# Kernel optimization log

Hardware: AMD Instinct MI355X
Metric: run time of the kernel (lower is better)

## Reference

```python
import jax, jax.numpy as jnp
import numpy as np

# EISANI constants (inference path, dense non-EI weights, static connections)
NUM_BITS = 16        # EISANITABcontinuousVarEncodingNumBits
K_SYN = 32           # numberOfSynapsesPerSegment
SEGMENTS = 2         # numberOfSegmentsPerNeuron
THETA = 8            # segment activation threshold (synapse-count based)
H = 4096             # hiddenLayerSize
F = 128              # numberOfFeatures
C = 10               # numberOfClasses
B = 64               # batch


def _make_weight(key, h, s, p):
    """Dense weight [h, s, p] with exactly K_SYN nonzero +/-1 synapses per segment
    (mirrors _initialise_layer_weights dense non-EI branch)."""
    k1, k2 = jax.random.split(key)
    cols = jax.random.randint(k1, (h, s, K_SYN), 0, p)
    signs = jnp.where(jax.random.bernoulli(k2, 0.5, (h, s, K_SYN)), 1.0, -1.0).astype(jnp.float32)
    hh = jnp.arange(h)[:, None, None]
    ss = jnp.arange(s)[None, :, None]
    return jnp.zeros((h, s, p), jnp.float32).at[hh, ss, cols].set(signs)


def setup_inputs() -> dict:
    key = jax.random.key(0)
    kx, k0, k1, k2, ko = jax.random.split(key, 5)
    x = jax.random.uniform(kx, (B, F), dtype=jnp.float32)
    W0 = _make_weight(k0, H, SEGMENTS, F * NUM_BITS)
    W1 = _make_weight(k1, H, SEGMENTS, H)
    W2 = _make_weight(k2, H, SEGMENTS, H)
    outW = jax.random.normal(ko, (3, H, C), dtype=jnp.float32) * 0.02
    return {"x": x, "W0": W0, "W1": W1, "W2": W2, "outW": outW}


def _encode(x):
    # thermometer (graded) encoding of continuous vars into NUM_BITS binary bits
    thresholds = (jnp.arange(NUM_BITS, dtype=jnp.float32) + 1.0) / (NUM_BITS + 1.0)
    bits = (x[:, :, None] >= thresholds).astype(jnp.float32)  # [B, F, NUM_BITS]
    return bits.reshape(x.shape[0], -1)  # [B, F*NUM_BITS]


def reference(x, W0, W1, W2, outW):
    acts = _encode(x)  # [B, P0]
    layer_acts = []
    for W in (W0, W1, W2):
        # segment membrane sums over binary presynaptic activations
        z = jnp.einsum('bp,hsp->bhs', acts, W)  # [B, H, S]
        # neuron fires if ANY segment reaches threshold
        fired = jnp.any(z >= THETA, axis=-1)
        acts = fired.astype(jnp.float32)  # binary activation [B, H]
        layer_acts.append(acts)
    stacked = jnp.stack(layer_acts)  # [L, B, H]
    out = jnp.einsum('lbh,lhc->bc', stacked, outW)  # class scores [B, C]
    return out
```

## Files before the change

kernel.cpp:

```cpp
#include <hip/hip_runtime.h>
#include <hip/hip_bf16.h>

typedef unsigned long long u64;
typedef float f32x4 __attribute__((ext_vector_type(4)));

#define H_SZ 4096
#define NBITS 16
#define NFEAT 128
#define NCLS 10
#define THETA 8


__device__ __forceinline__ u64 bfly_stage(u64 x, int lane, int d, u64 Md) {
    u64 p = __shfl_xor(x, d);
    return (lane & d) ? ((x & Md) | ((p >> d) & ~Md))
                      : ((x & ~Md) | ((p << d) & Md));
}

__device__ __forceinline__ u64 transpose64(u64 x, int lane) {
    x = bfly_stage(x, lane, 32, 0xFFFFFFFF00000000ULL);
    x = bfly_stage(x, lane, 16, 0xFFFF0000FFFF0000ULL);
    x = bfly_stage(x, lane,  8, 0xFF00FF00FF00FF00ULL);
    x = bfly_stage(x, lane,  4, 0xF0F0F0F0F0F0F0F0ULL);
    x = bfly_stage(x, lane,  2, 0xCCCCCCCCCCCCCCCCULL);
    x = bfly_stage(x, lane,  1, 0xAAAAAAAAAAAAAAAAULL);
    return x;
}

__device__ __forceinline__ void chunk_accum(f32x4 a, f32x4 b, const u64* p,
                                            unsigned& zp0, unsigned& zn0,
                                            unsigned& zp1, unsigned& zn1) {
    u64 A0 = p[0], A1 = p[64], A2 = p[128], A3 = p[192];
    u64 m;
    m = __ballot(a.x > 0.0f); zp0 += __builtin_popcountll(A0 & m);
    m = __ballot(a.x < 0.0f); zn0 += __builtin_popcountll(A0 & m);
    m = __ballot(a.y > 0.0f); zp0 += __builtin_popcountll(A1 & m);
    m = __ballot(a.y < 0.0f); zn0 += __builtin_popcountll(A1 & m);
    m = __ballot(a.z > 0.0f); zp0 += __builtin_popcountll(A2 & m);
    m = __ballot(a.z < 0.0f); zn0 += __builtin_popcountll(A2 & m);
    m = __ballot(a.w > 0.0f); zp0 += __builtin_popcountll(A3 & m);
    m = __ballot(a.w < 0.0f); zn0 += __builtin_popcountll(A3 & m);

    m = __ballot(b.x > 0.0f); zp1 += __builtin_popcountll(A0 & m);
    m = __ballot(b.x < 0.0f); zn1 += __builtin_popcountll(A0 & m);
    m = __ballot(b.y > 0.0f); zp1 += __builtin_popcountll(A1 & m);
    m = __ballot(b.y < 0.0f); zn1 += __builtin_popcountll(A1 & m);
    m = __ballot(b.z > 0.0f); zp1 += __builtin_popcountll(A2 & m);
    m = __ballot(b.z < 0.0f); zn1 += __builtin_popcountll(A2 & m);
    m = __ballot(b.w > 0.0f); zp1 += __builtin_popcountll(A3 & m);
    m = __ballot(b.w < 0.0f); zn1 += __builtin_popcountll(A3 & m);
}

template <int NC>
__device__ __forceinline__ u64 layer_accum(const f32x4* w0, const f32x4* w1,
                                           const f32x4 pa[4], const f32x4 pb[4],
                                           const u64* lds, int lane) {
    unsigned zp0 = 0, zn0 = 0, zp1 = 0, zn1 = 0;
    #pragma unroll
    for (int c = 0; c < 4; c++)
        chunk_accum(pa[c], pb[c], lds + c * 256 + lane, zp0, zn0, zp1, zn1);
    #pragma unroll 4
    for (int c = 4; c < NC; c++) {
        f32x4 a = __builtin_nontemporal_load(w0 + c * 64);
        f32x4 b = __builtin_nontemporal_load(w1 + c * 64);
        chunk_accum(a, b, lds + c * 256 + lane, zp0, zn0, zp1, zn1);
    }
    int z0 = (int)zp0 - (int)zn0;
    int z1 = (int)zp1 - (int)zn1;
    return __ballot(z0 >= THETA) | __ballot(z1 >= THETA);
}

__global__ __launch_bounds__(256, 4) void layer0_kernel(
    const float* __restrict__ x, const float* __restrict__ W0,
    u64* __restrict__ fired0, float* __restrict__ out, int out_n)
{
    __shared__ __align__(16) u64 lds[32 * 64];
    int tid = threadIdx.x;
    int lane = tid & 63;
    int warp = tid >> 6;
    int h = blockIdx.x * 4 + warp;

    const f32x4* w0 = (const f32x4*)(W0 + (size_t)(2 * h) * 2048) + lane;
    const f32x4* w1 = (const f32x4*)(W0 + (size_t)(2 * h + 1) * 2048) + lane;
    f32x4 pa[4], pb[4];
    #pragma unroll
    for (int c = 0; c < 4; c++) {
        pa[c] = __builtin_nontemporal_load(w0 + c * 64);
        pb[c] = __builtin_nontemporal_load(w1 + c * 64);
    }

    if (blockIdx.x == 0)
        for (int i = tid; i < out_n; i += 256)
            out[i] = 0.0f;

    {
        float thr0 = (4 * 0 + warp + 1.0f) / (NBITS + 1.0f);
        float thr1 = (4 * 1 + warp + 1.0f) / (NBITS + 1.0f);
        float thr2 = (4 * 2 + warp + 1.0f) / (NBITS + 1.0f);
        float thr3 = (4 * 3 + warp + 1.0f) / (NBITS + 1.0f);
        const f32x4* xb = (const f32x4*)(x + lane * NFEAT);
        #pragma unroll
        for (int c = 0; c < 8; c++) {
            u64 word = 0;
            #pragma unroll
            for (int q = 0; q < 4; q++) {
                f32x4 v = xb[c * 4 + q];
                int base = q * 16;
                word |= (u64)(v.x >= thr0) << (base + 0);
                word |= (u64)(v.x >= thr1) << (base + 1);
                word |= (u64)(v.x >= thr2) << (base + 2);
                word |= (u64)(v.x >= thr3) << (base + 3);
                word |= (u64)(v.y >= thr0) << (base + 4);
                word |= (u64)(v.y >= thr1) << (base + 5);
                word |= (u64)(v.y >= thr2) << (base + 6);
                word |= (u64)(v.y >= thr3) << (base + 7);
                word |= (u64)(v.z >= thr0) << (base + 8);
                word |= (u64)(v.z >= thr1) << (base + 9);
                word |= (u64)(v.z >= thr2) << (base + 10);
                word |= (u64)(v.z >= thr3) << (base + 11);
                word |= (u64)(v.w >= thr0) << (base + 12);
                word |= (u64)(v.w >= thr1) << (base + 13);
                word |= (u64)(v.w >= thr2) << (base + 14);
                word |= (u64)(v.w >= thr3) << (base + 15);
            }
            lds[(c * 4 + warp) * 64 + lane] = word;
        }
    }
    __syncthreads();
    u64 f0 = layer_accum<8>(w0, w1, pa, pb, lds, lane);
    if (lane == 0) fired0[h] = f0;
}

__global__ __launch_bounds__(256, 4) void layerN_kernel(
    const float* __restrict__ W, const u64* __restrict__ fired_in,
    u64* __restrict__ fired_out)
{
    __shared__ __align__(16) u64 lds[64 * 64];
    int tid = threadIdx.x;
    int lane = tid & 63;
    int warp = tid >> 6;
    int h = blockIdx.x * 4 + warp;

    const f32x4* w0 = (const f32x4*)(W + (size_t)(2 * h) * 4096) + lane;
    const f32x4* w1 = (const f32x4*)(W + (size_t)(2 * h + 1) * 4096) + lane;
    f32x4 pa[4], pb[4];
    #pragma unroll
    for (int c = 0; c < 4; c++) {
        pa[c] = __builtin_nontemporal_load(w0 + c * 64);
        pb[c] = __builtin_nontemporal_load(w1 + c * 64);
    }

    #pragma unroll 4
    for (int c = 0; c < 16; c++) {
        u64 xw = fired_in[c * 256 + 4 * lane + warp];
        xw = transpose64(xw, lane);
        lds[(c * 4 + warp) * 64 + lane] = xw;
    }
    __syncthreads();
    u64 f = layer_accum<16>(w0, w1, pa, pb, lds, lane);
    if (lane == 0) fired_out[h] = f;
}

__global__ void output_kernel(const float* __restrict__ outW,
                              const u64* __restrict__ fired,
                              float* __restrict__ out) {
    __shared__ float red[4][64];
    int tid = threadIdx.x;
    int lane = tid & 63;
    int warp = tid >> 6;
    int wid = blockIdx.x * 4 + warp;
    int l = wid / (NCLS * 64);
    int rem = wid % (NCLS * 64);
    int c = rem / 64;
    int chunk = rem % 64;
    const u64* fl = fired + l * H_SZ;
    int h0 = chunk * 64;
    float acc = 0.0f;
    #pragma unroll 8
    for (int h = h0; h < h0 + 64; h++) {
        float wv = outW[((size_t)(l * H_SZ + h)) * NCLS + c];
        if ((fl[h] >> lane) & 1ULL) acc += wv;
    }
    red[warp][lane] = acc;
    __syncthreads();
    if (warp == 0) {
        float s = red[0][lane] + red[1][lane] + red[2][lane] + red[3][lane];
        atomicAdd(&out[lane * NCLS + c], s);
    }
}

extern "C" void kernel_launch(void* const* d_in, const int* in_sizes, int n_in,
                              void* d_out, int out_size, void* d_ws, size_t ws_size,
                              hipStream_t stream) {
    const float* x    = (const float*)d_in[0];
    const float* W0   = (const float*)d_in[1];
    const float* W1   = (const float*)d_in[2];
    const float* W2   = (const float*)d_in[3];
    const float* outW = (const float*)d_in[4];
    float* out = (float*)d_out;

    u64* fired = (u64*)d_ws;

    layer0_kernel<<<1024, 256, 0, stream>>>(x, W0, fired, out, out_size);
    layerN_kernel<<<1024, 256, 0, stream>>>(W1, fired, fired + H_SZ);
    layerN_kernel<<<1024, 256, 0, stream>>>(W2, fired + H_SZ, fired + 2 * H_SZ);
    output_kernel<<<480, 256, 0, stream>>>(outW, fired, out);
}
```

Measured before the change: 357.7 us.

## Fuse all layers and output into one persistent kernel with grid barriers

Merges the four kernel launches into one persistent kernel of 1024 blocks that uses atomic-counter grid barriers between layers. It prefetches the next layer's first weight chunks before each barrier to overlap loads with the wait, and encodes the input once into workspace instead of once per block. This removes launch gaps and tail effects between kernels. In exchange it adds a memset, atomic spin barriers, and depends on all 1024 blocks being co-resident (4 per CU), or the kernel deadlocks.

```diff
diff --git a/kernel.cpp b/kernel.cpp
--- a/kernel.cpp
+++ b/kernel.cpp
@@ -1,5 +1,4 @@
 #include <hip/hip_runtime.h>
-#include <hip/hip_bf16.h>
 
 typedef unsigned long long u64;
 typedef float f32x4 __attribute__((ext_vector_type(4)));
@@ -9,6 +8,7 @@
 #define NFEAT 128
 #define NCLS 10
 #define THETA 8
+#define NBLK 1024
 
 
 __device__ __forceinline__ u64 bfly_stage(u64 x, int lane, int d, u64 Md) {
@@ -25,6 +25,17 @@
     x = bfly_stage(x, lane,  2, 0xCCCCCCCCCCCCCCCCULL);
     x = bfly_stage(x, lane,  1, 0xAAAAAAAAAAAAAAAAULL);
     return x;
+}
+
+__device__ __forceinline__ void grid_barrier(unsigned* cnt, unsigned goal, int tid) {
+    __syncthreads();
+    if (tid == 0) {
+        __hip_atomic_fetch_add(cnt, 1u, __ATOMIC_RELEASE, __HIP_MEMORY_SCOPE_AGENT);
+        while (__hip_atomic_load(cnt, __ATOMIC_RELAXED, __HIP_MEMORY_SCOPE_AGENT) < goal)
+            __builtin_amdgcn_s_sleep(1);
+        __threadfence();
+    }
+    __syncthreads();
 }
 
 __device__ __forceinline__ void chunk_accum(f32x4 a, f32x4 b, const u64* p,
@@ -70,16 +81,24 @@
     return __ballot(z0 >= THETA) | __ballot(z1 >= THETA);
 }
 
-__global__ __launch_bounds__(256, 4) void layer0_kernel(
-    const float* __restrict__ x, const float* __restrict__ W0,
-    u64* __restrict__ fired0, float* __restrict__ out, int out_n)
+__global__ __launch_bounds__(256, 4) void eisani_kernel(
+    const float* __restrict__ x,  const float* __restrict__ W0,
+    const float* __restrict__ W1, const float* __restrict__ W2,
+    const float* __restrict__ outW, u64* __restrict__ fired,
+    u64* __restrict__ actp0, unsigned* __restrict__ cnt,
+    float* __restrict__ out, int out_n)
 {
-    __shared__ __align__(16) u64 lds[32 * 64];
+    __shared__ __align__(16) u64 lds[64 * 64];
+    __shared__ float red[4][64];
     int tid = threadIdx.x;
     int lane = tid & 63;
     int warp = tid >> 6;
     int h = blockIdx.x * 4 + warp;
 
+    u64* fired0 = fired;
+    u64* fired1 = fired + H_SZ;
+    u64* fired2 = fired + 2 * H_SZ;
+
     const f32x4* w0 = (const f32x4*)(W0 + (size_t)(2 * h) * 2048) + lane;
     const f32x4* w1 = (const f32x4*)(W0 + (size_t)(2 * h + 1) * 2048) + lane;
     f32x4 pa[4], pb[4];
@@ -88,104 +107,99 @@
         pa[c] = __builtin_nontemporal_load(w0 + c * 64);
         pb[c] = __builtin_nontemporal_load(w1 + c * 64);
     }
-
     if (blockIdx.x == 0)
-        for (int i = tid; i < out_n; i += 256)
-            out[i] = 0.0f;
+        for (int i = tid; i < out_n; i += 256) out[i] = 0.0f;
+    if (blockIdx.x < 8) {
+        int idx = blockIdx.x * 256 + tid;
+        int wword = idx >> 6, b = idx & 63;
+        int cc = wword >> 2, j = wword & 3;
+        float thr0 = (4 * 0 + j + 1.0f) / (NBITS + 1.0f);
+        float thr1 = (4 * 1 + j + 1.0f) / (NBITS + 1.0f);
+        float thr2 = (4 * 2 + j + 1.0f) / (NBITS + 1.0f);
+        float thr3 = (4 * 3 + j + 1.0f) / (NBITS + 1.0f);
+        const float* xb = x + b * NFEAT + cc * 16;
+        u64 word = 0;
+        #pragma unroll
+        for (int k = 0; k < 16; k++) {
+            float xv = xb[k];
+            word |= (u64)(xv >= thr0) << (4 * k + 0);
+            word |= (u64)(xv >= thr1) << (4 * k + 1);
+            word |= (u64)(xv >= thr2) << (4 * k + 2);
+            word |= (u64)(xv >= thr3) << (4 * k + 3);
+        }
+        actp0[wword * 64 + b] = word;
+    }
+    grid_barrier(cnt, 1 * NBLK, tid);
 
     {
-        float thr0 = (4 * 0 + warp + 1.0f) / (NBITS + 1.0f);
-        float thr1 = (4 * 1 + warp + 1.0f) / (NBITS + 1.0f);
-        float thr2 = (4 * 2 + warp + 1.0f) / (NBITS + 1.0f);
-        float thr3 = (4 * 3 + warp + 1.0f) / (NBITS + 1.0f);
-        const f32x4* xb = (const f32x4*)(x + lane * NFEAT);
-        #pragma unroll
-        for (int c = 0; c < 8; c++) {
-            u64 word = 0;
-            #pragma unroll
-            for (int q = 0; q < 4; q++) {
-                f32x4 v = xb[c * 4 + q];
-                int base = q * 16;
-                word |= (u64)(v.x >= thr0) << (base + 0);
-                word |= (u64)(v.x >= thr1) << (base + 1);
-                word |= (u64)(v.x >= thr2) << (base + 2);
-                word |= (u64)(v.x >= thr3) << (base + 3);
-                word |= (u64)(v.y >= thr0) << (base + 4);
-                word |= (u64)(v.y >= thr1) << (base + 5);
-                word |= (u64)(v.y >= thr2) << (base + 6);
-                word |= (u64)(v.y >= thr3) << (base + 7);
-                word |= (u64)(v.z >= thr0) << (base + 8);
-                word |= (u64)(v.z >= thr1) << (base + 9);
-                word |= (u64)(v.z >= thr2) << (base + 10);
-                word |= (u64)(v.z >= thr3) << (base + 11);
-                word |= (u64)(v.w >= thr0) << (base + 12);
-                word |= (u64)(v.w >= thr1) << (base + 13);
-                word |= (u64)(v.w >= thr2) << (base + 14);
-                word |= (u64)(v.w >= thr3) << (base + 15);
-            }
-            lds[(c * 4 + warp) * 64 + lane] = word;
-        }
-    }
-    __syncthreads();
-    u64 f0 = layer_accum<8>(w0, w1, pa, pb, lds, lane);
-    if (lane == 0) fired0[h] = f0;
-}
-
-__global__ __launch_bounds__(256, 4) void layerN_kernel(
-    const float* __restrict__ W, const u64* __restrict__ fired_in,
-    u64* __restrict__ fired_out)
-{
-    __shared__ __align__(16) u64 lds[64 * 64];
-    int tid = threadIdx.x;
-    int lane = tid & 63;
-    int warp = tid >> 6;
-    int h = blockIdx.x * 4 + warp;
-
-    const f32x4* w0 = (const f32x4*)(W + (size_t)(2 * h) * 4096) + lane;
-    const f32x4* w1 = (const f32x4*)(W + (size_t)(2 * h + 1) * 4096) + lane;
-    f32x4 pa[4], pb[4];
+        const ulonglong2* src = (const ulonglong2*)actp0;
+        ulonglong2* dst = (ulonglong2*)lds;
+        for (int i = tid; i < 1024; i += 256) dst[i] = src[i];
+    }
+    __syncthreads();
+    u64 fv = layer_accum<8>(w0, w1, pa, pb, lds, lane);
+    if (lane == 0) fired0[h] = fv;
+
+    w0 = (const f32x4*)(W1 + (size_t)(2 * h) * 4096) + lane;
+    w1 = (const f32x4*)(W1 + (size_t)(2 * h + 1) * 4096) + lane;
     #pragma unroll
     for (int c = 0; c < 4; c++) {
         pa[c] = __builtin_nontemporal_load(w0 + c * 64);
         pb[c] = __builtin_nontemporal_load(w1 + c * 64);
     }
+    grid_barrier(cnt, 2 * NBLK, tid);
 
     #pragma unroll 4
     for (int c = 0; c < 16; c++) {
-        u64 xw = fired_in[c * 256 + 4 * lane + warp];
+        u64 xw = fired0[c * 256 + 4 * lane + warp];
         xw = transpose64(xw, lane);
         lds[(c * 4 + warp) * 64 + lane] = xw;
     }
     __syncthreads();
-    u64 f = layer_accum<16>(w0, w1, pa, pb, lds, lane);
-    if (lane == 0) fired_out[h] = f;
-}
-
-__global__ void output_kernel(const float* __restrict__ outW,
-                              const u64* __restrict__ fired,
-                              float* __restrict__ out) {
-    __shared__ float red[4][64];
-    int tid = threadIdx.x;
-    int lane = tid & 63;
-    int warp = tid >> 6;
-    int wid = blockIdx.x * 4 + warp;
-    int l = wid / (NCLS * 64);
-    int rem = wid % (NCLS * 64);
-    int c = rem / 64;
-    int chunk = rem % 64;
-    const u64* fl = fired + l * H_SZ;
-    int h0 = chunk * 64;
-    float acc = 0.0f;
-    #pragma unroll 8
-    for (int h = h0; h < h0 + 64; h++) {
-        float wv = outW[((size_t)(l * H_SZ + h)) * NCLS + c];
-        if ((fl[h] >> lane) & 1ULL) acc += wv;
-    }
-    red[warp][lane] = acc;
-    __syncthreads();
-    if (warp == 0) {
-        float s = red[0][lane] + red[1][lane] + red[2][lane] + red[3][lane];
-        atomicAdd(&out[lane * NCLS + c], s);
+    fv = layer_accum<16>(w0, w1, pa, pb, lds, lane);
+    if (lane == 0) fired1[h] = fv;
+
+    w0 = (const f32x4*)(W2 + (size_t)(2 * h) * 4096) + lane;
+    w1 = (const f32x4*)(W2 + (size_t)(2 * h + 1) * 4096) + lane;
+    #pragma unroll
+    for (int c = 0; c < 4; c++) {
+        pa[c] = __builtin_nontemporal_load(w0 + c * 64);
+        pb[c] = __builtin_nontemporal_load(w1 + c * 64);
+    }
+    grid_barrier(cnt, 3 * NBLK, tid);
+
+    #pragma unroll 4
+    for (int c = 0; c < 16; c++) {
+        u64 xw = fired1[c * 256 + 4 * lane + warp];
+        xw = transpose64(xw, lane);
+        lds[(c * 4 + warp) * 64 + lane] = xw;
+    }
+    __syncthreads();
+    fv = layer_accum<16>(w0, w1, pa, pb, lds, lane);
+    if (lane == 0) fired2[h] = fv;
+
+    grid_barrier(cnt, 4 * NBLK, tid);
+
+    if (blockIdx.x < 480) {
+        int wid = blockIdx.x * 4 + warp;
+        int l = wid / (NCLS * 64);
+        int rem = wid % (NCLS * 64);
+        int c = rem / 64;
+        int chunk = rem % 64;
+        const u64* fl = fired + l * H_SZ;
+        int h0 = chunk * 64;
+        float acc = 0.0f;
+        #pragma unroll 8
+        for (int hh = h0; hh < h0 + 64; hh++) {
+            float wv = outW[((size_t)(l * H_SZ + hh)) * NCLS + c];
+            if ((fl[hh] >> lane) & 1ULL) acc += wv;
+        }
+        red[warp][lane] = acc;
+        __syncthreads();
+        if (warp == 0) {
+            float s = red[0][lane] + red[1][lane] + red[2][lane] + red[3][lane];
+            atomicAdd(&out[lane * NCLS + c], s);
+        }
     }
 }
 
@@ -199,10 +213,13 @@
     const float* outW = (const float*)d_in[4];
     float* out = (float*)d_out;
 
-    u64* fired = (u64*)d_ws;
-
-    layer0_kernel<<<1024, 256, 0, stream>>>(x, W0, fired, out, out_size);
-    layerN_kernel<<<1024, 256, 0, stream>>>(W1, fired, fired + H_SZ);
-    layerN_kernel<<<1024, 256, 0, stream>>>(W2, fired + H_SZ, fired + 2 * H_SZ);
-    output_kernel<<<480, 256, 0, stream>>>(outW, fired, out);
-}
+    char* ws = (char*)d_ws;
+    u64* fired      = (u64*)(ws);
+    u64* actp0      = (u64*)(ws + 98304);
+    unsigned* cnt   = (unsigned*)(ws + 114688);
+
+    hipMemsetAsync(cnt, 0, 128, stream);
+
+    eisani_kernel<<<NBLK, 256, 0, stream>>>(x, W0, W1, W2, outW,
+                                            fired, actp0, cnt, out, out_size);
+}
```

Result: slower. 779.4 us (+117.9%).
